# Optimization experiments

Measured on AMD Instinct MI355X. Metric: run time of the kernel, lower is better.

Reference implementation:

```python
import jax, jax.numpy as jnp
import numpy as np

N_VOX = 100000
GRID = 128
C_IN = 64
C_OUT = 64
EPS = 1e-5


def _build_sparse_voxels():
    rng = np.random.default_rng(0)
    lin = rng.choice(GRID ** 3, size=N_VOX, replace=False).astype(np.int64)
    z = lin // (GRID * GRID)
    y = (lin // GRID) % GRID
    x = lin % GRID
    coords = np.stack([z, y, x], axis=1)  # [N,3]
    lookup = np.full(GRID ** 3, -1, dtype=np.int32)
    lookup[lin] = np.arange(N_VOX, dtype=np.int32)
    offs = np.stack(np.meshgrid(*[np.arange(-1, 2)] * 3, indexing='ij'), -1).reshape(27, 3)
    nb = coords[:, None, :] + offs[None, :, :]  # [N,27,3]
    valid = np.all((nb >= 0) & (nb < GRID), axis=-1)
    nb_lin = nb[..., 0] * GRID * GRID + nb[..., 1] * GRID + nb[..., 2]
    nb_lin = np.clip(nb_lin, 0, GRID ** 3 - 1)
    nb_idx = np.where(valid, lookup[nb_lin], -1).astype(np.int32)  # [N,27], -1 = missing
    return nb_idx


def setup_inputs() -> dict:
    key = jax.random.key(0)
    k1, k2, k3, k4, k5 = jax.random.split(key, 5)
    nb_idx = jnp.asarray(_build_sparse_voxels())
    return {
        'feats': jax.random.normal(k1, (N_VOX, C_IN), jnp.float32),
        'neighbor_idx': nb_idx,
        'W_conv': jax.random.normal(k2, (27, C_IN, C_OUT), jnp.float32) * 0.05,
        'b_conv': jax.random.normal(k3, (C_OUT,), jnp.float32) * 0.05,
        'W_lin': jax.random.normal(k4, (C_OUT, C_OUT), jnp.float32) * 0.05,
        'b_lin': jax.random.normal(k5, (C_OUT,), jnp.float32) * 0.05,
        'gamma': jnp.ones((C_OUT,), jnp.float32),
        'beta': jnp.zeros((C_OUT,), jnp.float32),
    }


def reference(feats, neighbor_idx, W_conv, b_conv, W_lin, b_lin, gamma, beta):
    # Submanifold sparse conv3d: gather active neighbors per kernel offset,
    # contract with per-offset weights, scatter back to the same active sites.
    mask = (neighbor_idx >= 0)
    safe_idx = jnp.where(mask, neighbor_idx, 0)
    gathered = feats[safe_idx] * mask[..., None].astype(feats.dtype)  # [N,27,Cin]
    x = jnp.einsum('nkc,kcd->nd', gathered, W_conv) + b_conv  # [N,Cout]
    # Linear
    x = x @ W_lin + b_lin
    # LayerNorm over channel dim
    mu = jnp.mean(x, axis=-1, keepdims=True)
    var = jnp.mean(jnp.square(x - mu), axis=-1, keepdims=True)
    return gamma * (x - mu) * jax.lax.rsqrt(var + EPS) + beta
```

## Files before the change

kernel.cpp:

```cpp
#include <hip/hip_runtime.h>
#include <hip/hip_bf16.h>

#define KOFF 27
#define C 64
#define EPS 1e-5f
#define BR 128
#define STCAP 256
#define STP 68
#define RLW_L 12

typedef __attribute__((ext_vector_type(8))) short short8;
typedef __attribute__((ext_vector_type(4))) float f32x4;

__device__ inline unsigned short f2bf(float x) {
    __hip_bfloat16 h = __float2bfloat16(x);
    unsigned short u;
    __builtin_memcpy(&u, &h, 2);
    return u;
}
__device__ inline float bf2f(unsigned short u) {
    unsigned int t = ((unsigned int)u) << 16;
    float f;
    __builtin_memcpy(&f, &t, 4);
    return f;
}

__launch_bounds__(256)
__global__ void prep(const float* __restrict__ feats,
                     const float* __restrict__ Wc, const float* __restrict__ Wl,
                     unsigned short* __restrict__ feats_bf, unsigned short* __restrict__ WcF,
                     unsigned short* __restrict__ WlF, unsigned short* __restrict__ Z,
                     int nvox, int nblk_f) {
    const int b = blockIdx.x;
    const int tid = threadIdx.x;

    if (b < nblk_f) {
        const int n4 = nvox * 16;
        const int stride = nblk_f * 256;
        for (int i = b * 256 + tid; i < n4; i += stride) {
            float4 v = ((const float4*)feats)[i];
            ushort4 u;
            u.x = f2bf(v.x); u.y = f2bf(v.y); u.z = f2bf(v.z); u.w = f2bf(v.w);
            ((ushort4*)feats_bf)[i] = u;
        }
    } else {
        const int NWc = KOFF * 4096;
        int i = (b - nblk_f) * 256 + tid;
        if (i < NWc + 4096) {
            int rem = i & 4095;
            int t = rem >> 10;
            int ks = (rem >> 9) & 1;
            int l = (rem >> 3) & 63;
            int j = i & 7;
            int c = ks * 32 + ((l >> 4) << 3) + j;
            int d = (t << 4) + (l & 15);
            if (i < NWc) {
                int ko = i >> 12;
                WcF[i] = f2bf(Wc[(ko << 12) + (c << 6) + d]);
            } else {
                WlF[rem] = f2bf(Wl[(c << 6) + d]);
            }
        } else if (i < NWc + 4096 + 128) {
            Z[i - NWc - 4096] = 0;
        }
    }
}

struct SM {
    union {
        int nb[BR * KOFF];
        unsigned short st[STCAP * STP];
    } u;
    int pairs[STCAP];
    short rowlist[BR][RLW_L];
    unsigned char rowcnt2[BR];
    int cnt[KOFF];
    int sb[KOFF];
    int wcnt[KOFF][2];
    int table[224];
    int T;
};

__launch_bounds__(256)
__global__ void fused(const unsigned short* __restrict__ feats,
                      const int* __restrict__ nb,
                      const unsigned short* __restrict__ WcF,
                      const unsigned short* __restrict__ WlF,
                      const unsigned short* __restrict__ zpage,
                      const float* __restrict__ b_conv,
                      const float* __restrict__ b_lin,
                      const float* __restrict__ gamma,
                      const float* __restrict__ beta,
                      float* __restrict__ out, int nvox) {
    __shared__ SM sm;
    const int tid = threadIdx.x;
    const int lane = tid & 63;
    const int wave = tid >> 6;
    const int m = lane & 15;
    const int krow = lane >> 4;
    const int coff = krow * 8;
    const int row0 = blockIdx.x * BR;

    {
        const long gb = (long)row0 * KOFF;
        const long glim = (long)nvox * KOFF;
        for (int j = tid; j < BR * KOFF; j += 256) {
            long g = gb + j;
            sm.u.nb[j] = (g < glim) ? nb[g] : -1;
        }
    }
    __syncthreads();

    if (tid < BR) {
#pragma unroll
        for (int ko = 0; ko < KOFF; ++ko) {
            if (ko == 13) continue;
            int src = sm.u.nb[tid * KOFF + ko];
            unsigned long long msk = __ballot(src >= 0);
            if (lane == 0) sm.wcnt[ko][wave] = __popcll(msk);
        }
    }
    __syncthreads();

    if (wave == 0) {
        int c = (lane < KOFF && lane != 13) ? (sm.wcnt[lane][0] + sm.wcnt[lane][1]) : 0;
        int incl = c;
#pragma unroll
        for (int d = 1; d < 32; d <<= 1) {
            int v = __shfl_up(incl, d, 64);
            if (lane >= d) incl += v;
        }
        if (lane < KOFF) { sm.cnt[lane] = c; sm.sb[lane] = incl - c; }
        int T = 0;
        for (int ko = 0; ko < KOFF; ++ko) {
            int ck = __shfl(c, ko, 64);
            for (int s0 = 0; s0 < ck; s0 += 16) {
                if (lane == 0) sm.table[T] = (ko << 16) | s0;
                ++T;
            }
        }
        if (lane == 0) sm.T = T;
    }
    __syncthreads();

    if (tid < BR) {
        const unsigned long long lmask = (1ull << lane) - 1;
        int j = 0;
#pragma unroll
        for (int ko = 0; ko < KOFF; ++ko) {
            if (ko == 13) continue;
            int src = sm.u.nb[tid * KOFF + ko];
            unsigned long long msk = __ballot(src >= 0);
            int pre = __popcll(msk & lmask);
            if (src >= 0) {
                int pos = sm.sb[ko] + ((wave == 1) ? sm.wcnt[ko][0] : 0) + pre;
                if (pos < STCAP) {
                    sm.pairs[pos] = src;
                    if (j < RLW_L) sm.rowlist[tid][j] = (short)pos;
                    ++j;
                }
            }
        }
        sm.rowcnt2[tid] = (unsigned char)((j < RLW_L) ? j : RLW_L);
    }
    __syncthreads();

    const int T = sm.T;
    for (int t = wave; t < T; t += 4) {
        int e = sm.table[t];
        int ko = e >> 16;
        int s0 = e & 0xFFFF;
        int cko = sm.cnt[ko];
        int sb = sm.sb[ko];

        int slot = s0 + m;
        int src = (slot < cko && sb + slot < STCAP) ? sm.pairs[sb + slot] : -1;
        const unsigned short* pa = (src >= 0) ? feats + ((size_t)src << 6) : zpage;
        short8 a0 = *(const short8*)(pa + coff);
        short8 a1 = *(const short8*)(pa + 32 + coff);

        const unsigned short* w = WcF + ((size_t)ko << 12) + lane * 8;
        f32x4 c4[4];
#pragma unroll
        for (int t4 = 0; t4 < 4; ++t4) {
            short8 b0 = *(const short8*)(w + t4 * 1024);
            short8 b1 = *(const short8*)(w + t4 * 1024 + 512);
            c4[t4] = (f32x4){0.f, 0.f, 0.f, 0.f};
            c4[t4] = __builtin_amdgcn_mfma_f32_16x16x32_bf16(a0, b0, c4[t4], 0, 0, 0);
            c4[t4] = __builtin_amdgcn_mfma_f32_16x16x32_bf16(a1, b1, c4[t4], 0, 0, 0);
        }
#pragma unroll
        for (int i = 0; i < 4; ++i) {
            int row16 = krow * 4 + i;
            int sr = sb + s0 + row16;
            if (s0 + row16 < cko && sr < STCAP) {
                ushort4 stv;
                stv.x = f2bf(c4[0][i]); stv.y = f2bf(c4[1][i]);
                stv.z = f2bf(c4[2][i]); stv.w = f2bf(c4[3][i]);
                *(ushort4*)&sm.u.st[sr * STP + m * 4] = stv;
            }
        }
    }
    __syncthreads();

    const int rl0 = wave * 32;
    const int gr0 = row0 + rl0;
    int r0c = min(gr0 + m, nvox - 1);
    int r1c = min(gr0 + 16 + m, nvox - 1);
    short8 a00 = *(const short8*)(feats + (size_t)r0c * C + coff);
    short8 a01 = *(const short8*)(feats + (size_t)r0c * C + 32 + coff);
    short8 a10 = *(const short8*)(feats + (size_t)r1c * C + coff);
    short8 a11 = *(const short8*)(feats + (size_t)r1c * C + 32 + coff);

    f32x4 cc0[4], cc1[4];
#pragma unroll
    for (int t = 0; t < 4; ++t) {
        cc0[t] = (f32x4){0.f, 0.f, 0.f, 0.f};
        cc1[t] = (f32x4){0.f, 0.f, 0.f, 0.f};
    }
#pragma unroll
    for (int rbk = 0; rbk < 2; ++rbk) {
        f32x4* cc = rbk ? cc1 : cc0;
#pragma unroll
        for (int i = 0; i < 4; ++i) {
            int rloc = rl0 + rbk * 16 + krow * 4 + i;
            int ncon = sm.rowcnt2[rloc];
            for (int jj = 0; jj < ncon; ++jj) {
                int idx = sm.rowlist[rloc][jj];
                ushort4 v = *(const ushort4*)&sm.u.st[idx * STP + m * 4];
                cc[0][i] += bf2f(v.x); cc[1][i] += bf2f(v.y);
                cc[2][i] += bf2f(v.z); cc[3][i] += bf2f(v.w);
            }
        }
    }
    const unsigned short* w13 = WcF + 13 * 4096 + lane * 8;
#pragma unroll
    for (int t = 0; t < 4; ++t) {
        short8 b0 = *(const short8*)(w13 + t * 1024);
        short8 b1 = *(const short8*)(w13 + t * 1024 + 512);
        cc0[t] = __builtin_amdgcn_mfma_f32_16x16x32_bf16(a00, b0, cc0[t], 0, 0, 0);
        cc0[t] = __builtin_amdgcn_mfma_f32_16x16x32_bf16(a01, b1, cc0[t], 0, 0, 0);
        cc1[t] = __builtin_amdgcn_mfma_f32_16x16x32_bf16(a10, b0, cc1[t], 0, 0, 0);
        cc1[t] = __builtin_amdgcn_mfma_f32_16x16x32_bf16(a11, b1, cc1[t], 0, 0, 0);
    }
    __syncthreads();

    float bc[4], bl[4], g4[4], bt[4];
#pragma unroll
    for (int t = 0; t < 4; ++t) {
        int col = t * 16 + m;
        bc[t] = b_conv[col];
        bl[t] = b_lin[col];
        g4[t] = gamma[col];
        bt[t] = beta[col];
    }
    unsigned short* xl = sm.u.st + wave * 16 * 72;

    for (int rbk = 0; rbk < 2; ++rbk) {
        f32x4* cc = rbk ? cc1 : cc0;
#pragma unroll
        for (int t = 0; t < 4; ++t)
#pragma unroll
            for (int i = 0; i < 4; ++i)
                xl[(krow * 4 + i) * 72 + t * 16 + m] = f2bf(cc[t][i] + bc[t]);

        short8 xa0 = *(const short8*)&xl[m * 72 + coff];
        short8 xa1 = *(const short8*)&xl[m * 72 + 32 + coff];

        f32x4 d[4];
#pragma unroll
        for (int t = 0; t < 4; ++t) d[t] = (f32x4){0.f, 0.f, 0.f, 0.f};
        const unsigned short* wl = WlF + lane * 8;
#pragma unroll
        for (int t = 0; t < 4; ++t) {
            short8 wb0 = *(const short8*)(wl + t * 1024);
            short8 wb1 = *(const short8*)(wl + t * 1024 + 512);
            d[t] = __builtin_amdgcn_mfma_f32_16x16x32_bf16(xa0, wb0, d[t], 0, 0, 0);
            d[t] = __builtin_amdgcn_mfma_f32_16x16x32_bf16(xa1, wb1, d[t], 0, 0, 0);
        }

        float s1[4], s2[4];
#pragma unroll
        for (int i = 0; i < 4; ++i) {
            float q0 = d[0][i] + bl[0];
            float q1 = d[1][i] + bl[1];
            float q2 = d[2][i] + bl[2];
            float q3 = d[3][i] + bl[3];
            d[0][i] = q0; d[1][i] = q1; d[2][i] = q2; d[3][i] = q3;
            s1[i] = q0 + q1 + q2 + q3;
            s2[i] = q0 * q0 + q1 * q1 + q2 * q2 + q3 * q3;
        }
#pragma unroll
        for (int msk = 1; msk < 16; msk <<= 1) {
#pragma unroll
            for (int i = 0; i < 4; ++i) {
                s1[i] += __shfl_xor(s1[i], msk, 64);
                s2[i] += __shfl_xor(s2[i], msk, 64);
            }
        }
#pragma unroll
        for (int i = 0; i < 4; ++i) {
            float mu = s1[i] * (1.f / 64.f);
            float var = s2[i] * (1.f / 64.f) - mu * mu;
            float rs = rsqrtf(var + EPS);
            int grow = gr0 + rbk * 16 + krow * 4 + i;
            if (grow < nvox) {
#pragma unroll
                for (int t = 0; t < 4; ++t)
                    out[(size_t)grow * C + t * 16 + m] = g4[t] * (d[t][i] - mu) * rs + bt[t];
            }
        }
    }
}

extern "C" void kernel_launch(void* const* d_in, const int* in_sizes, int n_in,
                              void* d_out, int out_size, void* d_ws, size_t ws_size,
                              hipStream_t stream) {
    const float* feats = (const float*)d_in[0];
    const int* nb = (const int*)d_in[1];
    const float* Wc = (const float*)d_in[2];
    const float* b_conv = (const float*)d_in[3];
    const float* Wl = (const float*)d_in[4];
    const float* b_lin = (const float*)d_in[5];
    const float* gamma = (const float*)d_in[6];
    const float* beta = (const float*)d_in[7];
    float* out = (float*)d_out;

    const int nvox = in_sizes[0] / C;

    char* ws = (char*)d_ws;
    unsigned short* feats_bf = (unsigned short*)ws;
    size_t off = (size_t)nvox * C * 2;
    unsigned short* WcF = (unsigned short*)(ws + off); off += KOFF * 4096 * 2;
    unsigned short* WlF = (unsigned short*)(ws + off); off += 4096 * 2;
    unsigned short* Z = (unsigned short*)(ws + off);   off += 256;

    const int NBF = 1024;
    const int NBW = (KOFF * 4096 + 4096 + 128 + 255) / 256;
    prep<<<NBF + NBW, 256, 0, stream>>>(feats, Wc, Wl, feats_bf, WcF, WlF, Z, nvox, NBF);

    int nblk = (nvox + BR - 1) / BR;
    fused<<<nblk, 256, 0, stream>>>(feats_bf, nb, WcF, WlF, Z,
                                    b_conv, b_lin, gamma, beta, out, nvox);
}
```

Before: 50.65 us.

## Move neighbor-pair list construction into prep kernel and stream metadata to fused kernel

```diff
diff --git a/kernel.cpp b/kernel.cpp
--- a/kernel.cpp
+++ b/kernel.cpp
@@ -8,6 +8,7 @@
 #define STCAP 256
 #define STP 68
 #define RLW_L 12
+#define META 280
 
 typedef __attribute__((ext_vector_type(8))) short short8;
 typedef __attribute__((ext_vector_type(4))) float f32x4;
@@ -25,19 +26,108 @@
     return f;
 }
 
+struct SMB {
+    int nb[BR * KOFF];
+    int pairs[STCAP];
+    short rowlist[BR][RLW_L];
+    unsigned char rowcnt2[BR];
+    int cnt[KOFF];
+    int sb[KOFF];
+    int wcnt[KOFF][2];
+    int table[224];
+    int T;
+};
+
 __launch_bounds__(256)
-__global__ void prep(const float* __restrict__ feats,
-                     const float* __restrict__ Wc, const float* __restrict__ Wl,
-                     unsigned short* __restrict__ feats_bf, unsigned short* __restrict__ WcF,
-                     unsigned short* __restrict__ WlF, unsigned short* __restrict__ Z,
-                     int nvox, int nblk_f) {
+__global__ void prep_build(const float* __restrict__ feats, const int* __restrict__ nb,
+                           const float* __restrict__ Wc, const float* __restrict__ Wl,
+                           unsigned short* __restrict__ feats_bf,
+                           unsigned short* __restrict__ WcF,
+                           unsigned short* __restrict__ WlF, unsigned short* __restrict__ Z,
+                           int* __restrict__ gmeta, int* __restrict__ gpairs,
+                           short* __restrict__ growlist, unsigned char* __restrict__ growcnt,
+                           int nvox, int nblk_b, int nblk_f) {
+    __shared__ SMB sm;
     const int b = blockIdx.x;
     const int tid = threadIdx.x;
 
-    if (b < nblk_f) {
+    if (b < nblk_b) {
+        const int lane = tid & 63;
+        const int wave = tid >> 6;
+        const int row0 = b * BR;
+        {
+            const long gb = (long)row0 * KOFF;
+            const long glim = (long)nvox * KOFF;
+            for (int j = tid; j < BR * KOFF; j += 256) {
+                long g = gb + j;
+                sm.nb[j] = (g < glim) ? nb[g] : -1;
+            }
+        }
+        __syncthreads();
+        if (tid < BR) {
+#pragma unroll
+            for (int ko = 0; ko < KOFF; ++ko) {
+                if (ko == 13) continue;
+                int src = sm.nb[tid * KOFF + ko];
+                unsigned long long msk = __ballot(src >= 0);
+                if (lane == 0) sm.wcnt[ko][wave] = __popcll(msk);
+            }
+        }
+        __syncthreads();
+        if (wave == 0) {
+            int c = (lane < KOFF && lane != 13) ? (sm.wcnt[lane][0] + sm.wcnt[lane][1]) : 0;
+            int incl = c;
+#pragma unroll
+            for (int d = 1; d < 32; d <<= 1) {
+                int v = __shfl_up(incl, d, 64);
+                if (lane >= d) incl += v;
+            }
+            if (lane < KOFF) { sm.cnt[lane] = c; sm.sb[lane] = incl - c; }
+            int T = 0;
+            for (int ko = 0; ko < KOFF; ++ko) {
+                int ck = __shfl(c, ko, 64);
+                for (int s0 = 0; s0 < ck; s0 += 16) {
+                    if (lane == 0) sm.table[T] = (ko << 16) | s0;
+                    ++T;
+                }
+            }
+            if (lane == 0) sm.T = T;
+        }
+        __syncthreads();
+        if (tid < BR) {
+            const unsigned long long lmask = (1ull << lane) - 1;
+            int j = 0;
+#pragma unroll
+            for (int ko = 0; ko < KOFF; ++ko) {
+                if (ko == 13) continue;
+                int src = sm.nb[tid * KOFF + ko];
+                unsigned long long msk = __ballot(src >= 0);
+                int pre = __popcll(msk & lmask);
+                if (src >= 0) {
+                    int pos = sm.sb[ko] + ((wave == 1) ? sm.wcnt[ko][0] : 0) + pre;
+                    if (pos < STCAP) {
+                        sm.pairs[pos] = src;
+                        if (j < RLW_L) sm.rowlist[tid][j] = (short)pos;
+                        ++j;
+                    }
+                }
+            }
+            sm.rowcnt2[tid] = (unsigned char)((j < RLW_L) ? j : RLW_L);
+        }
+        __syncthreads();
+        int* meta = gmeta + (size_t)b * META;
+        if (tid < KOFF) { meta[tid] = sm.cnt[tid]; meta[27 + tid] = sm.sb[tid]; }
+        if (tid == 0) meta[54] = sm.T;
+        for (int j = tid; j < 224; j += 256) meta[55 + j] = sm.table[j];
+        for (int j = tid; j < STCAP; j += 256) gpairs[(size_t)b * STCAP + j] = sm.pairs[j];
+        const short* rl = (const short*)sm.rowlist;
+        for (int j = tid; j < BR * RLW_L; j += 256)
+            growlist[(size_t)b * BR * RLW_L + j] = rl[j];
+        if (tid < BR) growcnt[(size_t)b * BR + tid] = sm.rowcnt2[tid];
+    } else if (b < nblk_b + nblk_f) {
         const int n4 = nvox * 16;
         const int stride = nblk_f * 256;
-        for (int i = b * 256 + tid; i < n4; i += stride) {
+        for (int i = (b - nblk_b) * 256 + tid; i < n4; i += stride) {
             float4 v = ((const float4*)feats)[i];
             ushort4 u;
             u.x = f2bf(v.x); u.y = f2bf(v.y); u.z = f2bf(v.z); u.w = f2bf(v.w);
@@ -45,7 +135,7 @@
         }
     } else {
         const int NWc = KOFF * 4096;
-        int i = (b - nblk_f) * 256 + tid;
+        int i = (b - nblk_b - nblk_f) * 256 + tid;
         if (i < NWc + 4096) {
             int rem = i & 4095;
             int t = rem >> 10;
@@ -66,33 +156,31 @@
     }
 }
 
-struct SM {
-    union {
-        int nb[BR * KOFF];
-        unsigned short st[STCAP * STP];
-    } u;
+struct SM2 {
+    unsigned short st[STCAP * STP];
     int pairs[STCAP];
     short rowlist[BR][RLW_L];
     unsigned char rowcnt2[BR];
     int cnt[KOFF];
     int sb[KOFF];
-    int wcnt[KOFF][2];
     int table[224];
     int T;
 };
 
 __launch_bounds__(256)
-__global__ void fused(const unsigned short* __restrict__ feats,
-                      const int* __restrict__ nb,
-                      const unsigned short* __restrict__ WcF,
-                      const unsigned short* __restrict__ WlF,
-                      const unsigned short* __restrict__ zpage,
-                      const float* __restrict__ b_conv,
-                      const float* __restrict__ b_lin,
-                      const float* __restrict__ gamma,
-                      const float* __restrict__ beta,
-                      float* __restrict__ out, int nvox) {
-    __shared__ SM sm;
+__global__ void fused2(const unsigned short* __restrict__ feats,
+                       const unsigned short* __restrict__ WcF,
+                       const unsigned short* __restrict__ WlF,
+                       const unsigned short* __restrict__ zpage,
+                       const int* __restrict__ gmeta, const int* __restrict__ gpairs,
+                       const short* __restrict__ growlist,
+                       const unsigned char* __restrict__ growcnt,
+                       const float* __restrict__ b_conv,
+                       const float* __restrict__ b_lin,
+                       const float* __restrict__ gamma,
+                       const float* __restrict__ beta,
+                       float* __restrict__ out, int nvox) {
+    __shared__ SM2 sm;
     const int tid = threadIdx.x;
     const int lane = tid & 63;
     const int wave = tid >> 6;
@@ -102,66 +190,16 @@
     const int row0 = blockIdx.x * BR;
 
     {
-        const long gb = (long)row0 * KOFF;
-        const long glim = (long)nvox * KOFF;
-        for (int j = tid; j < BR * KOFF; j += 256) {
-            long g = gb + j;
-            sm.u.nb[j] = (g < glim) ? nb[g] : -1;
-        }
-    }
-    __syncthreads();
-
-    if (tid < BR) {
-#pragma unroll
-        for (int ko = 0; ko < KOFF; ++ko) {
-            if (ko == 13) continue;
-            int src = sm.u.nb[tid * KOFF + ko];
-            unsigned long long msk = __ballot(src >= 0);
-            if (lane == 0) sm.wcnt[ko][wave] = __popcll(msk);
-        }
-    }
-    __syncthreads();
-
-    if (wave == 0) {
-        int c = (lane < KOFF && lane != 13) ? (sm.wcnt[lane][0] + sm.wcnt[lane][1]) : 0;
-        int incl = c;
-#pragma unroll
-        for (int d = 1; d < 32; d <<= 1) {
-            int v = __shfl_up(incl, d, 64);
-            if (lane >= d) incl += v;
-        }
-        if (lane < KOFF) { sm.cnt[lane] = c; sm.sb[lane] = incl - c; }
-        int T = 0;
-        for (int ko = 0; ko < KOFF; ++ko) {
-            int ck = __shfl(c, ko, 64);
-            for (int s0 = 0; s0 < ck; s0 += 16) {
-                if (lane == 0) sm.table[T] = (ko << 16) | s0;
-                ++T;
-            }
-        }
-        if (lane == 0) sm.T = T;
-    }
-    __syncthreads();
-
-    if (tid < BR) {
-        const unsigned long long lmask = (1ull << lane) - 1;
-        int j = 0;
-#pragma unroll
-        for (int ko = 0; ko < KOFF; ++ko) {
-            if (ko == 13) continue;
-            int src = sm.u.nb[tid * KOFF + ko];
-            unsigned long long msk = __ballot(src >= 0);
-            int pre = __popcll(msk & lmask);
-            if (src >= 0) {
-                int pos = sm.sb[ko] + ((wave == 1) ? sm.wcnt[ko][0] : 0) + pre;
-                if (pos < STCAP) {
-                    sm.pairs[pos] = src;
-                    if (j < RLW_L) sm.rowlist[tid][j] = (short)pos;
-                    ++j;
-                }
-            }
-        }
-        sm.rowcnt2[tid] = (unsigned char)((j < RLW_L) ? j : RLW_L);
+        const int* meta = gmeta + (size_t)blockIdx.x * META;
+        if (tid < KOFF) { sm.cnt[tid] = meta[tid]; sm.sb[tid] = meta[27 + tid]; }
+        if (tid == 0) sm.T = meta[54];
+        for (int j = tid; j < 224; j += 256) sm.table[j] = meta[55 + j];
+        for (int j = tid; j < STCAP; j += 256)
+            sm.pairs[j] = gpairs[(size_t)blockIdx.x * STCAP + j];
+        short* rl = (short*)sm.rowlist;
+        for (int j = tid; j < BR * RLW_L; j += 256)
+            rl[j] = growlist[(size_t)blockIdx.x * BR * RLW_L + j];
+        if (tid < BR) sm.rowcnt2[tid] = growcnt[(size_t)blockIdx.x * BR + tid];
     }
     __syncthreads();
 
@@ -197,7 +235,7 @@
                 ushort4 stv;
                 stv.x = f2bf(c4[0][i]); stv.y = f2bf(c4[1][i]);
                 stv.z = f2bf(c4[2][i]); stv.w = f2bf(c4[3][i]);
-                *(ushort4*)&sm.u.st[sr * STP + m * 4] = stv;
+                *(ushort4*)&sm.st[sr * STP + m * 4] = stv;
             }
         }
     }
@@ -227,7 +265,7 @@
             int ncon = sm.rowcnt2[rloc];
             for (int jj = 0; jj < ncon; ++jj) {
                 int idx = sm.rowlist[rloc][jj];
-                ushort4 v = *(const ushort4*)&sm.u.st[idx * STP + m * 4];
+                ushort4 v = *(const ushort4*)&sm.st[idx * STP + m * 4];
                 cc[0][i] += bf2f(v.x); cc[1][i] += bf2f(v.y);
                 cc[2][i] += bf2f(v.z); cc[3][i] += bf2f(v.w);
             }
@@ -254,7 +292,7 @@
         g4[t] = gamma[col];
         bt[t] = beta[col];
     }
-    unsigned short* xl = sm.u.st + wave * 16 * 72;
+    unsigned short* xl = sm.st + wave * 16 * 72;
 
     for (int rbk = 0; rbk < 2; ++rbk) {
         f32x4* cc = rbk ? cc1 : cc0;
@@ -327,6 +365,7 @@
     float* out = (float*)d_out;
 
     const int nvox = in_sizes[0] / C;
+    const int nblk_b = (nvox + BR - 1) / BR;
 
     char* ws = (char*)d_ws;
     unsigned short* feats_bf = (unsigned short*)ws;
@@ -334,12 +373,22 @@
     unsigned short* WcF = (unsigned short*)(ws + off); off += KOFF * 4096 * 2;
     unsigned short* WlF = (unsigned short*)(ws + off); off += 4096 * 2;
     unsigned short* Z = (unsigned short*)(ws + off);   off += 256;
+    off = (off + 255) & ~(size_t)255;
+    int* gmeta = (int*)(ws + off);                      off += (size_t)nblk_b * META * 4;
+    off = (off + 255) & ~(size_t)255;
+    int* gpairs = (int*)(ws + off);                     off += (size_t)nblk_b * STCAP * 4;
+    off = (off + 255) & ~(size_t)255;
+    short* growlist = (short*)(ws + off);               off += (size_t)nblk_b * BR * RLW_L * 2;
+    off = (off + 255) & ~(size_t)255;
+    unsigned char* growcnt = (unsigned char*)(ws + off); off += (size_t)nblk_b * BR;
 
     const int NBF = 1024;
     const int NBW = (KOFF * 4096 + 4096 + 128 + 255) / 256;
-    prep<<<NBF + NBW, 256, 0, stream>>>(feats, Wc, Wl, feats_bf, WcF, WlF, Z, nvox, NBF);
-
-    int nblk = (nvox + BR - 1) / BR;
-    fused<<<nblk, 256, 0, stream>>>(feats_bf, nb, WcF, WlF, Z,
-                                    b_conv, b_lin, gamma, beta, out, nvox);
-}
+    prep_build<<<nblk_b + NBF + NBW, 256, 0, stream>>>(
+        feats, nb, Wc, Wl, feats_bf, WcF, WlF, Z,
+        gmeta, gpairs, growlist, growcnt, nvox, nblk_b, NBF);
+
+    fused2<<<nblk_b, 256, 0, stream>>>(feats_bf, WcF, WlF, Z,
+                                       gmeta, gpairs, growlist, growcnt,
+                                       b_conv, b_lin, gamma, beta, out, nvox);
+}
```

Measured after the change: 52.58 us. +3.8%, slower.
